# Optimization experiments

Hardware: AMD Instinct MI355X
Metric: run time of the kernel (lower is better)

Reference implementation:

```python
import jax, jax.numpy as jnp
import numpy as np

B, K, G, C = 64, 4000, 200, 91
LAMBDA_BOX, LAMBDA_CLS, LAMBDA_OBJ = 5.0, 1.0, 1.0
EPS = 1e-9


def _make_boxes(key, lead_shape):
    k1, k2 = jax.random.split(key)
    tl = jax.random.uniform(k1, lead_shape + (2,)) * 0.7
    wh = jax.random.uniform(k2, lead_shape + (2,)) * 0.29 + 0.01
    return jnp.concatenate([tl, tl + wh], axis=-1)


def setup_inputs() -> dict:
    key = jax.random.key(0)
    ks = jax.random.split(key, 6)
    pred_boxes = _make_boxes(ks[0], (B, K))
    pred_obj_logits = jax.random.normal(ks[1], (B, K), dtype=jnp.float32)
    pred_cls_logits = jax.random.normal(ks[2], (B, K, C), dtype=jnp.float32)
    gt_boxes = _make_boxes(ks[3], (B, G))
    gt_labels = jax.random.randint(ks[4], (B, G), 0, C)
    n_gt = jax.random.randint(ks[5], (B,), 1, G + 1)
    gt_mask = jnp.arange(G)[None, :] < n_gt[:, None]
    return dict(pred_boxes=pred_boxes, pred_obj_logits=pred_obj_logits,
                pred_cls_logits=pred_cls_logits, gt_boxes=gt_boxes,
                gt_labels=gt_labels, gt_mask=gt_mask)


def _area(x):
    return jnp.clip(x[..., 2] - x[..., 0], 0.0) * jnp.clip(x[..., 3] - x[..., 1], 0.0)


def _pairwise_iou(a, b):
    # a: (K,4), b: (G,4) -> (K,G)
    tl = jnp.maximum(a[:, None, :2], b[None, :, :2])
    br = jnp.minimum(a[:, None, 2:], b[None, :, 2:])
    wh = jnp.clip(br - tl, 0.0)
    inter = wh[..., 0] * wh[..., 1]
    union = jnp.clip(_area(a)[:, None] + _area(b)[None, :] - inter, EPS)
    return inter / union


def _ciou_loss(pb, gb):
    # pb, gb: (M,4) matched pairs; elementwise CIoU loss = 1 - CIoU
    tl = jnp.maximum(pb[:, :2], gb[:, :2])
    br = jnp.minimum(pb[:, 2:], gb[:, 2:])
    wh = jnp.clip(br - tl, 0.0)
    inter = wh[:, 0] * wh[:, 1]
    iou = inter / jnp.clip(_area(pb) + _area(gb) - inter, EPS)
    px = (pb[:, 0] + pb[:, 2]) * 0.5
    py = (pb[:, 1] + pb[:, 3]) * 0.5
    tx = (gb[:, 0] + gb[:, 2]) * 0.5
    ty = (gb[:, 1] + gb[:, 3]) * 0.5
    rho2 = (px - tx) ** 2 + (py - ty) ** 2
    etl = jnp.minimum(pb[:, :2], gb[:, :2])
    ebr = jnp.maximum(pb[:, 2:], gb[:, 2:])
    c2 = jnp.clip((ebr[:, 0] - etl[:, 0]) ** 2 + (ebr[:, 1] - etl[:, 1]) ** 2, EPS)
    pw = jnp.clip(pb[:, 2] - pb[:, 0], EPS)
    ph = jnp.clip(pb[:, 3] - pb[:, 1], EPS)
    tw = jnp.clip(gb[:, 2] - gb[:, 0], EPS)
    th = jnp.clip(gb[:, 3] - gb[:, 1], EPS)
    v = (4.0 / jnp.pi ** 2) * (jnp.arctan(tw / th) - jnp.arctan(pw / ph)) ** 2
    alpha = jax.lax.stop_gradient(v / (1.0 - iou + v + EPS))  # torch.no_grad
    return 1.0 - (iou - rho2 / c2 - alpha * v)


def _greedy_match(iou0):
    # iou0: (K,G), invalid gt columns pre-masked to -1. Fixed min(K,G)-step
    # argmax-and-mask scan reproducing the torch greedy loop (break -> valid=False).
    Gd = iou0.shape[1]
    steps = min(iou0.shape[0], Gd)

    def step(m, _):
        flat = jnp.argmax(m)
        p = flat // Gd
        g = flat % Gd
        valid = m.reshape(-1)[flat] >= 0.0
        m2 = m.at[p, :].set(-1.0).at[:, g].set(-1.0)
        return jnp.where(valid, m2, m), (p, g, valid)

    _, (ps, gs, vs) = jax.lax.scan(step, iou0, None, length=steps)
    return ps, gs, vs


def _per_batch(pred_b, cls_b, gt_b, labels_b, mask_b):
    iou = jax.lax.stop_gradient(_pairwise_iou(pred_b, gt_b))  # matching is non-diff (.item() in torch)
    iou = jnp.where(mask_b[None, :], iou, -1.0)
    ps, gs, vs = _greedy_match(iou)
    vf = vs.astype(pred_b.dtype)
    n = jnp.sum(vf)
    denom = jnp.maximum(n, 1.0)
    pb = pred_b[ps]
    gb = gt_b[gs]
    lbox = jnp.sum(_ciou_loss(pb, gb) * vf) / denom
    logp = jax.nn.log_softmax(cls_b[ps], axis=-1)
    lce = -jnp.take_along_axis(logp, labels_b[gs][:, None], axis=1)[:, 0]
    lcls = jnp.sum(lce * vf) / denom
    obj_tgt = jnp.zeros((pred_b.shape[0],), pred_b.dtype).at[
        jnp.where(vs, ps, pred_b.shape[0])].set(1.0, mode='drop')
    return lbox, lcls, obj_tgt, n > 0.0


def reference(pred_boxes, pred_obj_logits, pred_cls_logits, gt_boxes, gt_labels, gt_mask):
    lbox_b, lcls_b, obj_tgt, has = jax.vmap(_per_batch)(
        pred_boxes, pred_cls_logits, gt_boxes, gt_labels, gt_mask)
    hf = has.astype(pred_boxes.dtype)
    nb = jnp.maximum(jnp.sum(hf), 1.0)
    loss_box = jnp.sum(lbox_b * hf) / nb
    loss_cls = jnp.sum(lcls_b * hf) / nb
    # BCEWithLogits(mean): softplus(x) - t*x
    loss_obj = jnp.mean(jax.nn.softplus(pred_obj_logits) - obj_tgt * pred_obj_logits)
    total = LAMBDA_BOX * loss_box + LAMBDA_CLS * loss_cls + LAMBDA_OBJ * loss_obj
    return total, loss_box, loss_cls, loss_obj
```

## Files before the change

kernel.cpp:

```cpp
#include <hip/hip_runtime.h>
#include <math.h>

#define B_ 64
#define K_ 4000
#define G_ 200
#define C_ 91
#define EPS_ 1e-9f
#define NW_ 16
#define DEPTH_ 32
typedef unsigned long long ull;

#define WS_FLAG 0
#define WS_PART 256
#define WS_TOP 327680

__device__ __forceinline__ float box_area(float4 a) {
#pragma clang fp contract(off)
  return fmaxf(a.z - a.x, 0.f) * fmaxf(a.w - a.y, 0.f);
}

__device__ __forceinline__ float iou_ab(float4 a, float aA, float4 b, float aB) {
#pragma clang fp contract(off)
  float tlx = fmaxf(a.x, b.x), tly = fmaxf(a.y, b.y);
  float brx = fminf(a.z, b.z), bry = fminf(a.w, b.w);
  float w = fmaxf(brx - tlx, 0.f), h = fmaxf(bry - tly, 0.f);
  float inter = w * h;
  float uni = fmaxf(aA + aB - inter, EPS_);
  return inter / uni;
}

__device__ __forceinline__ float ciou_loss(float4 p, float4 g) {
  float tlx = fmaxf(p.x, g.x), tly = fmaxf(p.y, g.y);
  float brx = fminf(p.z, g.z), bry = fminf(p.w, g.w);
  float w = fmaxf(brx - tlx, 0.f), h = fmaxf(bry - tly, 0.f);
  float inter = w * h;
  float areaP = fmaxf(p.z - p.x, 0.f) * fmaxf(p.w - p.y, 0.f);
  float areaG = fmaxf(g.z - g.x, 0.f) * fmaxf(g.w - g.y, 0.f);
  float iou = inter / fmaxf(areaP + areaG - inter, EPS_);
  float px = (p.x + p.z) * 0.5f, py = (p.y + p.w) * 0.5f;
  float tx = (g.x + g.z) * 0.5f, ty = (g.y + g.w) * 0.5f;
  float rho2 = (px - tx) * (px - tx) + (py - ty) * (py - ty);
  float ex = fmaxf(p.z, g.z) - fminf(p.x, g.x);
  float ey = fmaxf(p.w, g.w) - fminf(p.y, g.y);
  float c2 = fmaxf(ex * ex + ey * ey, EPS_);
  float pw = fmaxf(p.z - p.x, EPS_), ph = fmaxf(p.w - p.y, EPS_);
  float tw = fmaxf(g.z - g.x, EPS_), th = fmaxf(g.w - g.y, EPS_);
  float dat = atanf(tw / th) - atanf(pw / ph);
  float v = (4.0f / (float)(M_PI * M_PI)) * dat * dat;
  float alpha = v / ((1.f - iou) + v + EPS_);
  return 1.f - (iou - rho2 / c2 - alpha * v);
}

__global__ void kdetect(const unsigned char* m8, int* flag) {
  int b = threadIdx.x;
  int ok = 1;
  const unsigned char* r = m8 + b * G_;
  if (r[0] != 1) ok = 0;
  int seen0 = 0;
  for (int g = 0; g < G_; ++g) {
    unsigned char c = r[g];
    if (c > 1) { ok = 0; break; }
    if (c == 0) seen0 = 1;
    else if (seen0) { ok = 0; break; }
  }
  int all = __all(ok);
  if (b == 0) *flag = all ? 1 : 0;
}

__device__ __forceinline__ float block_sum(float v, float* s_red) {
  for (int off = 32; off > 0; off >>= 1) v += __shfl_xor(v, off);
  int lane = threadIdx.x & 63, wid = threadIdx.x >> 6;
  if (lane == 0) s_red[wid] = v;
  __syncthreads();
  float r = 0.f;
  if (wid == 0) {
    float t = (lane < NW_) ? s_red[lane] : 0.f;
    for (int off = 32; off > 0; off >>= 1) t += __shfl_xor(t, off);
    r = t;
  }
  __syncthreads();
  return r;
}

__device__ __forceinline__ void merge4_stage(ull& v0, ull& v1, ull& v2, ull& v3,
                                             int off) {
  ull w0 = __shfl_xor(v0, off), w1 = __shfl_xor(v1, off);
  ull w2 = __shfl_xor(v2, off), w3 = __shfl_xor(v3, off);
  ull t0 = v0 > w3 ? v0 : w3;
  ull t1 = v1 > w2 ? v1 : w2;
  ull t2 = v2 > w1 ? v2 : w1;
  ull t3 = v3 > w0 ? v3 : w0;
  ull x;
  if (t2 > t0) { x = t0; t0 = t2; t2 = x; }
  if (t3 > t1) { x = t1; t1 = t3; t3 = x; }
  if (t1 > t0) { x = t0; t0 = t1; t1 = x; }
  if (t3 > t2) { x = t2; t2 = t3; t3 = x; }
  v0 = t0; v1 = t1; v2 = t2; v3 = t3;
}

#define TOP4_INS(key, t0, t1, t2, t3)                   \
  if ((key) > t3) {                                     \
    t3 = (key);                                         \
    ull tmp_;                                           \
    if (t3 > t2) { tmp_ = t2; t2 = t3; t3 = tmp_; }     \
    if (t2 > t1) { tmp_ = t1; t1 = t2; t2 = tmp_; }     \
    if (t1 > t0) { tmp_ = t0; t0 = t1; t1 = tmp_; }     \
  }

__device__ __forceinline__ void rank_extract(ull t0, ull t1, ull t2, ull t3,
                                             ull* dst, int lane) {
  int r0 = 0, r1 = 0, r2 = 0, r3 = 0;
  for (int i = 0; i < 64; ++i) {
    ull o0 = __shfl(t0, i), o1 = __shfl(t1, i);
    ull o2 = __shfl(t2, i), o3 = __shfl(t3, i);
    r0 += (o0 > t0) + (o1 > t0) + (o2 > t0) + (o3 > t0);
    r1 += (o0 > t1) + (o1 > t1) + (o2 > t1) + (o3 > t1);
    r2 += (o0 > t2) + (o1 > t2) + (o2 > t2) + (o3 > t2);
    r3 += (o0 > t3) + (o1 > t3) + (o2 > t3) + (o3 > t3);
  }
  int cut = (t3 != 0ull) ? (r3 + 1) : 0x7FFFFFFF;
  int nc = (t0 != 0ull) + (t1 != 0ull) + (t2 != 0ull) + (t3 != 0ull);
  for (int off = 32; off > 0; off >>= 1) {
    int oc = __shfl_xor(cut, off);
    cut = (oc < cut) ? oc : cut;
    nc += __shfl_xor(nc, off);
  }
  const int Lf = (cut < DEPTH_) ? cut : DEPTH_;
  const int zstart = (Lf < nc) ? Lf : nc;
  if (t0 != 0ull && r0 < Lf) dst[r0] = t0;
  if (t1 != 0ull && r1 < Lf) dst[r1] = t1;
  if (t2 != 0ull && r2 < Lf) dst[r2] = t2;
  if (t3 != 0ull && r3 < Lf) dst[r3] = t3;
  for (int o = lane; o < DEPTH_; o += 64)
    if (o >= zstart) dst[o] = 0ull;
}

__global__ __launch_bounds__(1024) void kinit(const float* __restrict__ pred_boxes,
                                              const float* __restrict__ gt_boxes,
                                              const void* __restrict__ gt_mask,
                                              char* __restrict__ ws) {
  __shared__ float4 s_p[K_];
  const int blk = blockIdx.x;
  const int b = blk >> 3, oct = blk & 7;
  const int tid = threadIdx.x, lane = tid & 63, wid = tid >> 6;
  const int msk8 = *(const int*)(ws + WS_FLAG);
  const float4* p4 = (const float4*)pred_boxes + (size_t)b * K_;
  const float4* g4 = (const float4*)gt_boxes + (size_t)b * G_;

  for (int i = tid; i < K_; i += 1024) s_p[i] = p4[i];
  __syncthreads();

  const int base = oct * 25;
  const int colA = base + wid;
  const int colB = base + 16 + wid;
  const bool hasB = (wid < 9);
  ull* wtop = (ull*)(ws + WS_TOP);

  int vA, vB = 0;
  if (msk8) vA = ((const unsigned char*)gt_mask)[(size_t)b * G_ + colA] != 0;
  else      vA = ((const int*)gt_mask)[(size_t)b * G_ + colA] != 0;
  if (hasB) {
    if (msk8) vB = ((const unsigned char*)gt_mask)[(size_t)b * G_ + colB] != 0;
    else      vB = ((const int*)gt_mask)[(size_t)b * G_ + colB] != 0;
  }

  float4 gbA, gbB;
  float gAA = 0.f, gAB = 0.f;
  if (vA) { gbA = g4[colA]; gAA = box_area(gbA); }
  if (vB) { gbB = g4[colB]; gAB = box_area(gbB); }

  ull a0 = 0, a1 = 0, a2 = 0, a3 = 0;
  ull b0 = 0, b1 = 0, b2 = 0, b3 = 0;
  if (vA | vB) {
#pragma unroll 2
    for (int k = lane; k < K_; k += 64) {
      float4 pb = s_p[k];
      float ar = box_area(pb);
      if (vA) {
        float iou = iou_ab(pb, ar, gbA, gAA);
        ull e = ((ull)__float_as_uint(iou) << 12) | (ull)(4095 - k);
        TOP4_INS(e, a0, a1, a2, a3);
      }
      if (vB) {
        float iou = iou_ab(pb, ar, gbB, gAB);
        ull e = ((ull)__float_as_uint(iou) << 12) | (ull)(4095 - k);
        TOP4_INS(e, b0, b1, b2, b3);
      }
    }
  }
  {
    ull* dstA = wtop + ((size_t)b * G_ + colA) * DEPTH_;
    if (vA) rank_extract(a0, a1, a2, a3, dstA, lane);
    else    for (int o = lane; o < DEPTH_; o += 64) dstA[o] = 0ull;
  }
  if (hasB) {
    ull* dstB = wtop + ((size_t)b * G_ + colB) * DEPTH_;
    if (vB) rank_extract(b0, b1, b2, b3, dstB, lane);
    else    for (int o = lane; o < DEPTH_; o += 64) dstB[o] = 0ull;
  }
}

__global__ __launch_bounds__(1024) void kmerged(
    const float* __restrict__ pred_boxes, const float* __restrict__ obj_logits,
    const float* __restrict__ cls_logits, const float* __restrict__ gt_boxes,
    const int* __restrict__ gt_labels, char* __restrict__ ws) {
  __shared__ float s_gx[G_], s_gy[G_], s_gz[G_], s_gw[G_], s_garea[G_];
  __shared__ unsigned char s_rowused[4096];
  __shared__ ull s_toplist[G_][DEPTH_ + 1];
  __shared__ int s_mp[G_];
  __shared__ unsigned short s_mg[G_];
  __shared__ int s_cnt;
  __shared__ float s_red[NW_];
  const int b = blockIdx.x;
  const int tid = threadIdx.x, lane = tid & 63, wid = tid >> 6;
  const float4* p4 = (const float4*)pred_boxes + (size_t)b * K_;
  const float4* g4 = (const float4*)gt_boxes + (size_t)b * G_;
  const ull* wtop = (const ull*)(ws + WS_TOP);

  for (int g = tid; g < G_; g += 1024) {
    float4 gb = g4[g];
    s_gx[g] = gb.x; s_gy[g] = gb.y; s_gz[g] = gb.z; s_gw[g] = gb.w;
    s_garea[g] = box_area(gb);
  }
  for (int k = tid; k < 4096; k += 1024) s_rowused[k] = 0;
  for (int i = tid; i < G_ * DEPTH_; i += 1024)
    s_toplist[i / DEPTH_][i % DEPTH_] = wtop[((size_t)b * G_) * DEPTH_ + i];
  __syncthreads();

  if (wid == 0) {
    ull key0 = 0, key1 = 0, key2 = 0, key3 = 0;
    int ptr0 = DEPTH_, ptr1 = DEPTH_, ptr2 = DEPTH_, ptr3 = DEPTH_;
    int cloc = 0;
#define SLOTINIT(S)                                                        \
    { int col = S * 64 + lane;                                             \
      if (col < G_) {                                                      \
        ull h_ = s_toplist[col][0];                                        \
        if (h_ != 0ull) {                                                  \
          key##S = (h_ << 8) | (ull)(255 - col); ptr##S = 1; ++cloc; } } }
    SLOTINIT(0) SLOTINIT(1) SLOTINIT(2) SLOTINIT(3)
#undef SLOTINIT
    for (int off = 32; off > 0; off >>= 1) cloc += __shfl_xor(cloc, off);
    const int cnt = cloc;
    if (lane == 0) s_cnt = cnt;

    for (int step = 0; step < cnt;) {
      ull v0 = key0, v1 = key1, v2 = key2, v3 = key3, x;
      if (v1 > v0) { x = v0; v0 = v1; v1 = x; }
      if (v3 > v2) { x = v2; v2 = v3; v3 = x; }
      if (v2 > v0) { x = v0; v0 = v2; v2 = x; }
      if (v3 > v1) { x = v1; v1 = v3; v3 = x; }
      if (v2 > v1) { x = v1; v1 = v2; v2 = x; }
      merge4_stage(v0, v1, v2, v3, 32);
      merge4_stage(v0, v1, v2, v3, 16);
      merge4_stage(v0, v1, v2, v3, 8);
      merge4_stage(v0, v1, v2, v3, 4);
      merge4_stage(v0, v1, v2, v3, 2);
      merge4_stage(v0, v1, v2, v3, 1);
      const int P0 = 4095 - (int)((v0 >> 8) & 0xFFF), G0 = 255 - (int)(v0 & 0xFF);
      const int P1 = 4095 - (int)((v1 >> 8) & 0xFFF), G1 = 255 - (int)(v1 & 0xFF);
      const int P2 = 4095 - (int)((v2 >> 8) & 0xFFF), G2 = 255 - (int)(v2 & 0xFF);
      const int P3 = 4095 - (int)((v3 >> 8) & 0xFFF), G3 = 255 - (int)(v3 & 0xFF);
      const int lim = cnt - step;
      const bool a2 = (v1 != 0ull) && (P1 != P0) && (lim > 1);
      const bool a3 = a2 && (v2 != 0ull) && (P2 != P0) && (P2 != P1) && (lim > 2);
      const bool a4 = a3 && (v3 != 0ull) && (P3 != P0) && (P3 != P1) && (P3 != P2) && (lim > 3);
      const int nacc = 1 + (int)a2 + (int)a3 + (int)a4;
      if (lane == 0) {
        s_mp[step] = P0; s_mg[step] = (unsigned short)G0; s_rowused[P0] = 1;
        if (a2) { s_mp[step + 1] = P1; s_mg[step + 1] = (unsigned short)G1; s_rowused[P1] = 1; }
        if (a3) { s_mp[step + 2] = P2; s_mg[step + 2] = (unsigned short)G2; s_rowused[P2] = 1; }
        if (a4) { s_mp[step + 3] = P3; s_mg[step + 3] = (unsigned short)G3; s_rowused[P3] = 1; }
      }
      __builtin_amdgcn_wave_barrier();
      const int gA = G0, gB = a2 ? G1 : -1, gC = a3 ? G2 : -1, gD = a4 ? G3 : -1;
      const int pA = P0, pB = a2 ? P1 : -1, pC = a3 ? P2 : -1, pD = a4 ? P3 : -1;
      int need = 0;
#define DEMOTE(S)                                                           \
      { int col = S * 64 + lane; ull kk = key##S;                           \
        if (kk != 0ull) {                                                   \
          if (col == gA || col == gB || col == gC || col == gD) {           \
            key##S = 0ull;                                                  \
          } else {                                                          \
            int krow = 4095 - (int)((kk >> 8) & 0xFFF);                     \
            if (krow == pA || krow == pB || krow == pC || krow == pD) {     \
              ull nk = 0ull; int np = ptr##S;                               \
              while (np < DEPTH_) {                                         \
                ull e0 = s_toplist[col][np];                                \
                ull e1 = (np + 1 < DEPTH_) ? s_toplist[col][np + 1] : 0ull; \
                int pr0 = 4095 - (int)((e0 >> 12) & 0xFFF);                 \
                int pr1 = 4095 - (int)((e1 >> 12) & 0xFFF);                 \
                unsigned char u0 = s_rowused[pr0];                          \
                unsigned char u1 = s_rowused[pr1];                          \
                if (e0 == 0ull) { np = DEPTH_; break; }                     \
                if (!u0) { nk = (e0 << 8) | (ull)(255 - col); np += 1; break; } \
                if (e1 == 0ull) { np = DEPTH_; break; }                     \
                if (!u1) { nk = (e1 << 8) | (ull)(255 - col); np += 2; break; } \
                np += 2;                                                    \
              }                                                             \
              ptr##S = np; key##S = nk;                                     \
              if (nk == 0ull) need |= (1 << S); } } } }
      DEMOTE(0) DEMOTE(1) DEMOTE(2) DEMOTE(3)
#undef DEMOTE
      while (__any(need)) {
        unsigned long long bal = __ballot(need != 0);
        int src = (int)__builtin_ctzll(bal);
        int myslot = need ? __builtin_ctz(need) : 0;
        int slot = __shfl(myslot, src);
        int col = slot * 64 + src;
        float4 gb = make_float4(s_gx[col], s_gy[col], s_gz[col], s_gw[col]);
        float gA2 = s_garea[col];
        ull t0 = 0, t1 = 0, t2 = 0, t3 = 0;
#pragma unroll 2
        for (int k = lane; k < K_; k += 64) {
          if (!s_rowused[k]) {
            float4 pb = p4[k];
            float iou = iou_ab(pb, box_area(pb), gb, gA2);
            ull e = ((ull)__float_as_uint(iou) << 12) | (ull)(4095 - k);
            TOP4_INS(e, t0, t1, t2, t3);
          }
        }
        int r0 = 0, r1 = 0, r2 = 0, r3 = 0;
        for (int i = 0; i < 64; ++i) {
          ull o0 = __shfl(t0, i), o1 = __shfl(t1, i);
          ull o2 = __shfl(t2, i), o3 = __shfl(t3, i);
          r0 += (o0 > t0) + (o1 > t0) + (o2 > t0) + (o3 > t0);
          r1 += (o0 > t1) + (o1 > t1) + (o2 > t1) + (o3 > t1);
          r2 += (o0 > t2) + (o1 > t2) + (o2 > t2) + (o3 > t2);
          r3 += (o0 > t3) + (o1 > t3) + (o2 > t3) + (o3 > t3);
        }
        int cut = (t3 != 0ull) ? (r3 + 1) : 0x7FFFFFFF;
        int nc = (t0 != 0ull) + (t1 != 0ull) + (t2 != 0ull) + (t3 != 0ull);
        for (int off = 32; off > 0; off >>= 1) {
          int oc = __shfl_xor(cut, off);
          cut = (oc < cut) ? oc : cut;
          nc += __shfl_xor(nc, off);
        }
        const int Lf = (cut < DEPTH_) ? cut : DEPTH_;
        const int zstart = (Lf < nc) ? Lf : nc;
        if (t0 != 0ull && r0 < Lf) s_toplist[col][r0] = t0;
        if (t1 != 0ull && r1 < Lf) s_toplist[col][r1] = t1;
        if (t2 != 0ull && r2 < Lf) s_toplist[col][r2] = t2;
        if (t3 != 0ull && r3 < Lf) s_toplist[col][r3] = t3;
        for (int o = lane; o < DEPTH_; o += 64)
          if (o >= zstart) s_toplist[col][o] = 0ull;
        __builtin_amdgcn_wave_barrier();
        ull newhead = s_toplist[col][0];
        if (lane == src) {
          ull nk = (newhead << 8) | (ull)(255 - col);
          if (slot == 0) { key0 = nk; ptr0 = 1; }
          else if (slot == 1) { key1 = nk; ptr1 = 1; }
          else if (slot == 2) { key2 = nk; ptr2 = 1; }
          else { key3 = nk; ptr3 = 1; }
          need &= ~(1 << slot);
        }
        __builtin_amdgcn_wave_barrier();
      }
      step += nacc;
    }
  }
  __syncthreads();

  const int cnt = s_cnt;
  float lbox = 0.f, lcls = 0.f;
  for (int i = tid; i < cnt; i += 1024) {
    int p = s_mp[i], g = s_mg[i];
    float4 pb = p4[p];
    float4 gb = make_float4(s_gx[g], s_gy[g], s_gz[g], s_gw[g]);
    lbox += ciou_loss(pb, gb);
    int label = gt_labels[(size_t)b * G_ + g];
    const float* lg = cls_logits + ((size_t)b * K_ + p) * C_;
    float m = -1e30f;
    for (int cc = 0; cc < C_; ++cc) m = fmaxf(m, lg[cc]);
    float s = 0.f;
    for (int cc = 0; cc < C_; ++cc) s += expf(lg[cc] - m);
    lcls += (m + logf(s)) - lg[label];
  }
  float obj = 0.f;
  const float* ol = obj_logits + (size_t)b * K_;
  for (int k = tid; k < K_; k += 1024) {
    float x = ol[k];
    float sp = fmaxf(x, 0.f) + log1pf(expf(-fabsf(x)));
    if (s_rowused[k]) sp -= x;
    obj += sp;
  }
  lbox = block_sum(lbox, s_red);
  lcls = block_sum(lcls, s_red);
  obj = block_sum(obj, s_red);
  if (tid == 0) {
    float* partials = (float*)(ws + WS_PART);
    float n = (float)cnt;
    float denom = fmaxf(n, 1.f);
    partials[b * 4 + 0] = lbox / denom;
    partials[b * 4 + 1] = lcls / denom;
    partials[b * 4 + 2] = obj;
    partials[b * 4 + 3] = (n > 0.f) ? 1.f : 0.f;
  }
}

__global__ void kfinal(const char* __restrict__ ws, float* __restrict__ out) {
  int b = threadIdx.x;
  const float* partials = (const float*)(ws + WS_PART);
  float lb = partials[b * 4 + 0], lc = partials[b * 4 + 1];
  float ob = partials[b * 4 + 2], hf = partials[b * 4 + 3];
  float sb = lb * hf, sc = lc * hf, sh = hf, so = ob;
  for (int off = 32; off > 0; off >>= 1) {
    sb += __shfl_xor(sb, off);
    sc += __shfl_xor(sc, off);
    sh += __shfl_xor(sh, off);
    so += __shfl_xor(so, off);
  }
  if (b == 0) {
    float nb = fmaxf(sh, 1.f);
    float box = sb / nb, cls = sc / nb;
    float obj = so / (float)(B_ * K_);
    out[0] = 5.f * box + cls + obj;
    out[1] = box;
    out[2] = cls;
    out[3] = obj;
  }
}

extern "C" void kernel_launch(void* const* d_in, const int* in_sizes, int n_in,
                              void* d_out, int out_size, void* d_ws, size_t ws_size,
                              hipStream_t stream) {
  const float* pred_boxes = (const float*)d_in[0];
  const float* obj_logits = (const float*)d_in[1];
  const float* cls_logits = (const float*)d_in[2];
  const float* gt_boxes = (const float*)d_in[3];
  const int* gt_labels = (const int*)d_in[4];
  const void* gt_mask = d_in[5];
  float* out = (float*)d_out;
  char* ws = (char*)d_ws;

  hipLaunchKernelGGL(kdetect, dim3(1), dim3(64), 0, stream,
                     (const unsigned char*)gt_mask, (int*)(ws + WS_FLAG));
  hipLaunchKernelGGL(kinit, dim3(B_ * 8), dim3(1024), 0, stream,
                     pred_boxes, gt_boxes, gt_mask, ws);
  hipLaunchKernelGGL(kmerged, dim3(B_), dim3(1024), 0, stream,
                     pred_boxes, obj_logits, cls_logits, gt_boxes, gt_labels, ws);
  hipLaunchKernelGGL(kfinal, dim3(1), dim3(64), 0, stream, ws, out);
}
```

Before: 265.8 us.

## Split matching into single-wave kernel and separate wide epilogue kernel

The merged per-batch kernel is split in two. A 64-thread kernel runs the serial greedy matching and writes matches, the row-used mask and counts to workspace, and a separate 1024-thread kernel computes the CIoU, cross-entropy and objectness sums. The toplist now also keeps a parallel array of decoded row indices, so the demotion scan reads 16-bit rows instead of decoding 64-bit keys. The intent is to stop idling 15 waves during the serial matching phase and to make the demote walk cheaper. The cost is an extra launch plus a workspace round trip for the intermediate results.

```diff
diff --git a/kernel.cpp b/kernel.cpp
--- a/kernel.cpp
+++ b/kernel.cpp
@@ -12,6 +12,9 @@
 
 #define WS_FLAG 0
 #define WS_PART 256
+#define WS_CNT 1536
+#define WS_MATCH 2048
+#define WS_ROWUSED 53248
 #define WS_TOP 327680
 
 __device__ __forceinline__ float box_area(float4 a) {
@@ -200,172 +203,203 @@
   }
 }
 
-__global__ __launch_bounds__(1024) void kmerged(
-    const float* __restrict__ pred_boxes, const float* __restrict__ obj_logits,
-    const float* __restrict__ cls_logits, const float* __restrict__ gt_boxes,
-    const int* __restrict__ gt_labels, char* __restrict__ ws) {
+__global__ __launch_bounds__(64) void kmatch(const float* __restrict__ pred_boxes,
+                                             const float* __restrict__ gt_boxes,
+                                             char* __restrict__ ws) {
   __shared__ float s_gx[G_], s_gy[G_], s_gz[G_], s_gw[G_], s_garea[G_];
   __shared__ unsigned char s_rowused[4096];
-  __shared__ ull s_toplist[G_][DEPTH_ + 1];
+  __shared__ ull s_tlkey[G_][DEPTH_ + 1];
+  __shared__ unsigned short s_tlrow[G_][DEPTH_ + 1];
   __shared__ int s_mp[G_];
   __shared__ unsigned short s_mg[G_];
-  __shared__ int s_cnt;
-  __shared__ float s_red[NW_];
   const int b = blockIdx.x;
-  const int tid = threadIdx.x, lane = tid & 63, wid = tid >> 6;
+  const int lane = threadIdx.x;
   const float4* p4 = (const float4*)pred_boxes + (size_t)b * K_;
   const float4* g4 = (const float4*)gt_boxes + (size_t)b * G_;
   const ull* wtop = (const ull*)(ws + WS_TOP);
 
-  for (int g = tid; g < G_; g += 1024) {
+  for (int g = lane; g < G_; g += 64) {
     float4 gb = g4[g];
     s_gx[g] = gb.x; s_gy[g] = gb.y; s_gz[g] = gb.z; s_gw[g] = gb.w;
     s_garea[g] = box_area(gb);
   }
-  for (int k = tid; k < 4096; k += 1024) s_rowused[k] = 0;
-  for (int i = tid; i < G_ * DEPTH_; i += 1024)
-    s_toplist[i / DEPTH_][i % DEPTH_] = wtop[((size_t)b * G_) * DEPTH_ + i];
-  __syncthreads();
-
-  if (wid == 0) {
-    ull key0 = 0, key1 = 0, key2 = 0, key3 = 0;
-    int ptr0 = DEPTH_, ptr1 = DEPTH_, ptr2 = DEPTH_, ptr3 = DEPTH_;
-    int cloc = 0;
+  for (int k = lane; k < 4096; k += 64) s_rowused[k] = 0;
+  for (int i = lane; i < G_ * DEPTH_; i += 64) {
+    ull v = wtop[(size_t)b * G_ * DEPTH_ + i];
+    int col = i / DEPTH_, o = i % DEPTH_;
+    s_tlkey[col][o] = v;
+    s_tlrow[col][o] = v ? (unsigned short)(4095 - (int)((v >> 12) & 0xFFF))
+                        : (unsigned short)0xFFFF;
+  }
+  __builtin_amdgcn_wave_barrier();
+
+  ull key0 = 0, key1 = 0, key2 = 0, key3 = 0;
+  int ptr0 = DEPTH_, ptr1 = DEPTH_, ptr2 = DEPTH_, ptr3 = DEPTH_;
+  int cloc = 0;
 #define SLOTINIT(S)                                                        \
-    { int col = S * 64 + lane;                                             \
-      if (col < G_) {                                                      \
-        ull h_ = s_toplist[col][0];                                        \
-        if (h_ != 0ull) {                                                  \
-          key##S = (h_ << 8) | (ull)(255 - col); ptr##S = 1; ++cloc; } } }
-    SLOTINIT(0) SLOTINIT(1) SLOTINIT(2) SLOTINIT(3)
+  { int col = S * 64 + lane;                                               \
+    if (col < G_) {                                                        \
+      ull h_ = s_tlkey[col][0];                                            \
+      if (h_ != 0ull) {                                                    \
+        key##S = (h_ << 8) | (ull)(255 - col); ptr##S = 1; ++cloc; } } }
+  SLOTINIT(0) SLOTINIT(1) SLOTINIT(2) SLOTINIT(3)
 #undef SLOTINIT
-    for (int off = 32; off > 0; off >>= 1) cloc += __shfl_xor(cloc, off);
-    const int cnt = cloc;
-    if (lane == 0) s_cnt = cnt;
-
-    for (int step = 0; step < cnt;) {
-      ull v0 = key0, v1 = key1, v2 = key2, v3 = key3, x;
-      if (v1 > v0) { x = v0; v0 = v1; v1 = x; }
-      if (v3 > v2) { x = v2; v2 = v3; v3 = x; }
-      if (v2 > v0) { x = v0; v0 = v2; v2 = x; }
-      if (v3 > v1) { x = v1; v1 = v3; v3 = x; }
-      if (v2 > v1) { x = v1; v1 = v2; v2 = x; }
-      merge4_stage(v0, v1, v2, v3, 32);
-      merge4_stage(v0, v1, v2, v3, 16);
-      merge4_stage(v0, v1, v2, v3, 8);
-      merge4_stage(v0, v1, v2, v3, 4);
-      merge4_stage(v0, v1, v2, v3, 2);
-      merge4_stage(v0, v1, v2, v3, 1);
-      const int P0 = 4095 - (int)((v0 >> 8) & 0xFFF), G0 = 255 - (int)(v0 & 0xFF);
-      const int P1 = 4095 - (int)((v1 >> 8) & 0xFFF), G1 = 255 - (int)(v1 & 0xFF);
-      const int P2 = 4095 - (int)((v2 >> 8) & 0xFFF), G2 = 255 - (int)(v2 & 0xFF);
-      const int P3 = 4095 - (int)((v3 >> 8) & 0xFFF), G3 = 255 - (int)(v3 & 0xFF);
-      const int lim = cnt - step;
-      const bool a2 = (v1 != 0ull) && (P1 != P0) && (lim > 1);
-      const bool a3 = a2 && (v2 != 0ull) && (P2 != P0) && (P2 != P1) && (lim > 2);
-      const bool a4 = a3 && (v3 != 0ull) && (P3 != P0) && (P3 != P1) && (P3 != P2) && (lim > 3);
-      const int nacc = 1 + (int)a2 + (int)a3 + (int)a4;
-      if (lane == 0) {
-        s_mp[step] = P0; s_mg[step] = (unsigned short)G0; s_rowused[P0] = 1;
-        if (a2) { s_mp[step + 1] = P1; s_mg[step + 1] = (unsigned short)G1; s_rowused[P1] = 1; }
-        if (a3) { s_mp[step + 2] = P2; s_mg[step + 2] = (unsigned short)G2; s_rowused[P2] = 1; }
-        if (a4) { s_mp[step + 3] = P3; s_mg[step + 3] = (unsigned short)G3; s_rowused[P3] = 1; }
-      }
+  for (int off = 32; off > 0; off >>= 1) cloc += __shfl_xor(cloc, off);
+  const int cnt = cloc;
+
+  for (int step = 0; step < cnt;) {
+    ull v0 = key0, v1 = key1, v2 = key2, v3 = key3, x;
+    if (v1 > v0) { x = v0; v0 = v1; v1 = x; }
+    if (v3 > v2) { x = v2; v2 = v3; v3 = x; }
+    if (v2 > v0) { x = v0; v0 = v2; v2 = x; }
+    if (v3 > v1) { x = v1; v1 = v3; v3 = x; }
+    if (v2 > v1) { x = v1; v1 = v2; v2 = x; }
+    merge4_stage(v0, v1, v2, v3, 32);
+    merge4_stage(v0, v1, v2, v3, 16);
+    merge4_stage(v0, v1, v2, v3, 8);
+    merge4_stage(v0, v1, v2, v3, 4);
+    merge4_stage(v0, v1, v2, v3, 2);
+    merge4_stage(v0, v1, v2, v3, 1);
+    const int P0 = 4095 - (int)((v0 >> 8) & 0xFFF), G0 = 255 - (int)(v0 & 0xFF);
+    const int P1 = 4095 - (int)((v1 >> 8) & 0xFFF), G1 = 255 - (int)(v1 & 0xFF);
+    const int P2 = 4095 - (int)((v2 >> 8) & 0xFFF), G2 = 255 - (int)(v2 & 0xFF);
+    const int P3 = 4095 - (int)((v3 >> 8) & 0xFFF), G3 = 255 - (int)(v3 & 0xFF);
+    const int lim = cnt - step;
+    const bool a2 = (v1 != 0ull) && (P1 != P0) && (lim > 1);
+    const bool a3 = a2 && (v2 != 0ull) && (P2 != P0) && (P2 != P1) && (lim > 2);
+    const bool a4 = a3 && (v3 != 0ull) && (P3 != P0) && (P3 != P1) && (P3 != P2) && (lim > 3);
+    const int nacc = 1 + (int)a2 + (int)a3 + (int)a4;
+    if (lane == 0) {
+      s_mp[step] = P0; s_mg[step] = (unsigned short)G0; s_rowused[P0] = 1;
+      if (a2) { s_mp[step + 1] = P1; s_mg[step + 1] = (unsigned short)G1; s_rowused[P1] = 1; }
+      if (a3) { s_mp[step + 2] = P2; s_mg[step + 2] = (unsigned short)G2; s_rowused[P2] = 1; }
+      if (a4) { s_mp[step + 3] = P3; s_mg[step + 3] = (unsigned short)G3; s_rowused[P3] = 1; }
+    }
+    __builtin_amdgcn_wave_barrier();
+    const int gA = G0, gB = a2 ? G1 : -1, gC = a3 ? G2 : -1, gD = a4 ? G3 : -1;
+    const int pA = P0, pB = a2 ? P1 : -1, pC = a3 ? P2 : -1, pD = a4 ? P3 : -1;
+    int need = 0;
+#define DEMOTE(S)                                                           \
+    { int col = S * 64 + lane; ull kk = key##S;                             \
+      if (kk != 0ull) {                                                     \
+        if (col == gA || col == gB || col == gC || col == gD) {             \
+          key##S = 0ull;                                                    \
+        } else {                                                            \
+          int krow = 4095 - (int)((kk >> 8) & 0xFFF);                       \
+          if (krow == pA || krow == pB || krow == pC || krow == pD) {       \
+            ull nk = 0ull; int np = ptr##S;                                 \
+            while (np < DEPTH_) {                                           \
+              int r_ = s_tlrow[col][np];                                    \
+              if (r_ == 0xFFFF) { np = DEPTH_; break; }                     \
+              if (!s_rowused[r_]) {                                         \
+                nk = (s_tlkey[col][np] << 8) | (ull)(255 - col);            \
+                ++np; break;                                                \
+              }                                                             \
+              ++np;                                                         \
+            }                                                               \
+            ptr##S = np; key##S = nk;                                       \
+            if (nk == 0ull) need |= (1 << S); } } } }
+    DEMOTE(0) DEMOTE(1) DEMOTE(2) DEMOTE(3)
+#undef DEMOTE
+    while (__any(need)) {
+      unsigned long long bal = __ballot(need != 0);
+      int src = (int)__builtin_ctzll(bal);
+      int myslot = need ? __builtin_ctz(need) : 0;
+      int slot = __shfl(myslot, src);
+      int col = slot * 64 + src;
+      float4 gb = make_float4(s_gx[col], s_gy[col], s_gz[col], s_gw[col]);
+      float gA2 = s_garea[col];
+      ull t0 = 0, t1 = 0, t2 = 0, t3 = 0;
+#pragma unroll 2
+      for (int k = lane; k < K_; k += 64) {
+        if (!s_rowused[k]) {
+          float4 pb = p4[k];
+          float iou = iou_ab(pb, box_area(pb), gb, gA2);
+          ull e = ((ull)__float_as_uint(iou) << 12) | (ull)(4095 - k);
+          TOP4_INS(e, t0, t1, t2, t3);
+        }
+      }
+      int r0 = 0, r1 = 0, r2 = 0, r3 = 0;
+      for (int i = 0; i < 64; ++i) {
+        ull o0 = __shfl(t0, i), o1 = __shfl(t1, i);
+        ull o2 = __shfl(t2, i), o3 = __shfl(t3, i);
+        r0 += (o0 > t0) + (o1 > t0) + (o2 > t0) + (o3 > t0);
+        r1 += (o0 > t1) + (o1 > t1) + (o2 > t1) + (o3 > t1);
+        r2 += (o0 > t2) + (o1 > t2) + (o2 > t2) + (o3 > t2);
+        r3 += (o0 > t3) + (o1 > t3) + (o2 > t3) + (o3 > t3);
+      }
+      int cut = (t3 != 0ull) ? (r3 + 1) : 0x7FFFFFFF;
+      int nc = (t0 != 0ull) + (t1 != 0ull) + (t2 != 0ull) + (t3 != 0ull);
+      for (int off = 32; off > 0; off >>= 1) {
+        int oc = __shfl_xor(cut, off);
+        cut = (oc < cut) ? oc : cut;
+        nc += __shfl_xor(nc, off);
+      }
+      const int Lf = (cut < DEPTH_) ? cut : DEPTH_;
+      const int zstart = (Lf < nc) ? Lf : nc;
+      if (t0 != 0ull && r0 < Lf) {
+        s_tlkey[col][r0] = t0;
+        s_tlrow[col][r0] = (unsigned short)(4095 - (int)((t0 >> 12) & 0xFFF));
+      }
+      if (t1 != 0ull && r1 < Lf) {
+        s_tlkey[col][r1] = t1;
+        s_tlrow[col][r1] = (unsigned short)(4095 - (int)((t1 >> 12) & 0xFFF));
+      }
+      if (t2 != 0ull && r2 < Lf) {
+        s_tlkey[col][r2] = t2;
+        s_tlrow[col][r2] = (unsigned short)(4095 - (int)((t2 >> 12) & 0xFFF));
+      }
+      if (t3 != 0ull && r3 < Lf) {
+        s_tlkey[col][r3] = t3;
+        s_tlrow[col][r3] = (unsigned short)(4095 - (int)((t3 >> 12) & 0xFFF));
+      }
+      for (int o = lane; o < DEPTH_; o += 64)
+        if (o >= zstart) { s_tlkey[col][o] = 0ull; s_tlrow[col][o] = 0xFFFF; }
       __builtin_amdgcn_wave_barrier();
-      const int gA = G0, gB = a2 ? G1 : -1, gC = a3 ? G2 : -1, gD = a4 ? G3 : -1;
-      const int pA = P0, pB = a2 ? P1 : -1, pC = a3 ? P2 : -1, pD = a4 ? P3 : -1;
-      int need = 0;
-#define DEMOTE(S)                                                           \
-      { int col = S * 64 + lane; ull kk = key##S;                           \
-        if (kk != 0ull) {                                                   \
-          if (col == gA || col == gB || col == gC || col == gD) {           \
-            key##S = 0ull;                                                  \
-          } else {                                                          \
-            int krow = 4095 - (int)((kk >> 8) & 0xFFF);                     \
-            if (krow == pA || krow == pB || krow == pC || krow == pD) {     \
-              ull nk = 0ull; int np = ptr##S;                               \
-              while (np < DEPTH_) {                                         \
-                ull e0 = s_toplist[col][np];                                \
-                ull e1 = (np + 1 < DEPTH_) ? s_toplist[col][np + 1] : 0ull; \
-                int pr0 = 4095 - (int)((e0 >> 12) & 0xFFF);                 \
-                int pr1 = 4095 - (int)((e1 >> 12) & 0xFFF);                 \
-                unsigned char u0 = s_rowused[pr0];                          \
-                unsigned char u1 = s_rowused[pr1];                          \
-                if (e0 == 0ull) { np = DEPTH_; break; }                     \
-                if (!u0) { nk = (e0 << 8) | (ull)(255 - col); np += 1; break; } \
-                if (e1 == 0ull) { np = DEPTH_; break; }                     \
-                if (!u1) { nk = (e1 << 8) | (ull)(255 - col); np += 2; break; } \
-                np += 2;                                                    \
-              }                                                             \
-              ptr##S = np; key##S = nk;                                     \
-              if (nk == 0ull) need |= (1 << S); } } } }
-      DEMOTE(0) DEMOTE(1) DEMOTE(2) DEMOTE(3)
-#undef DEMOTE
-      while (__any(need)) {
-        unsigned long long bal = __ballot(need != 0);
-        int src = (int)__builtin_ctzll(bal);
-        int myslot = need ? __builtin_ctz(need) : 0;
-        int slot = __shfl(myslot, src);
-        int col = slot * 64 + src;
-        float4 gb = make_float4(s_gx[col], s_gy[col], s_gz[col], s_gw[col]);
-        float gA2 = s_garea[col];
-        ull t0 = 0, t1 = 0, t2 = 0, t3 = 0;
-#pragma unroll 2
-        for (int k = lane; k < K_; k += 64) {
-          if (!s_rowused[k]) {
-            float4 pb = p4[k];
-            float iou = iou_ab(pb, box_area(pb), gb, gA2);
-            ull e = ((ull)__float_as_uint(iou) << 12) | (ull)(4095 - k);
-            TOP4_INS(e, t0, t1, t2, t3);
-          }
-        }
-        int r0 = 0, r1 = 0, r2 = 0, r3 = 0;
-        for (int i = 0; i < 64; ++i) {
-          ull o0 = __shfl(t0, i), o1 = __shfl(t1, i);
-          ull o2 = __shfl(t2, i), o3 = __shfl(t3, i);
-          r0 += (o0 > t0) + (o1 > t0) + (o2 > t0) + (o3 > t0);
-          r1 += (o0 > t1) + (o1 > t1) + (o2 > t1) + (o3 > t1);
-          r2 += (o0 > t2) + (o1 > t2) + (o2 > t2) + (o3 > t2);
-          r3 += (o0 > t3) + (o1 > t3) + (o2 > t3) + (o3 > t3);
-        }
-        int cut = (t3 != 0ull) ? (r3 + 1) : 0x7FFFFFFF;
-        int nc = (t0 != 0ull) + (t1 != 0ull) + (t2 != 0ull) + (t3 != 0ull);
-        for (int off = 32; off > 0; off >>= 1) {
-          int oc = __shfl_xor(cut, off);
-          cut = (oc < cut) ? oc : cut;
-          nc += __shfl_xor(nc, off);
-        }
-        const int Lf = (cut < DEPTH_) ? cut : DEPTH_;
-        const int zstart = (Lf < nc) ? Lf : nc;
-        if (t0 != 0ull && r0 < Lf) s_toplist[col][r0] = t0;
-        if (t1 != 0ull && r1 < Lf) s_toplist[col][r1] = t1;
-        if (t2 != 0ull && r2 < Lf) s_toplist[col][r2] = t2;
-        if (t3 != 0ull && r3 < Lf) s_toplist[col][r3] = t3;
-        for (int o = lane; o < DEPTH_; o += 64)
-          if (o >= zstart) s_toplist[col][o] = 0ull;
-        __builtin_amdgcn_wave_barrier();
-        ull newhead = s_toplist[col][0];
-        if (lane == src) {
-          ull nk = (newhead << 8) | (ull)(255 - col);
-          if (slot == 0) { key0 = nk; ptr0 = 1; }
-          else if (slot == 1) { key1 = nk; ptr1 = 1; }
-          else if (slot == 2) { key2 = nk; ptr2 = 1; }
-          else { key3 = nk; ptr3 = 1; }
-          need &= ~(1 << slot);
-        }
-        __builtin_amdgcn_wave_barrier();
-      }
-      step += nacc;
+      ull newhead = s_tlkey[col][0];
+      if (lane == src) {
+        ull nk = (newhead << 8) | (ull)(255 - col);
+        if (slot == 0) { key0 = nk; ptr0 = 1; }
+        else if (slot == 1) { key1 = nk; ptr1 = 1; }
+        else if (slot == 2) { key2 = nk; ptr2 = 1; }
+        else { key3 = nk; ptr3 = 1; }
+        need &= ~(1 << slot);
+      }
+      __builtin_amdgcn_wave_barrier();
     }
-  }
-  __syncthreads();
-
-  const int cnt = s_cnt;
+    step += nacc;
+  }
+
+  unsigned* mout = (unsigned*)(ws + WS_MATCH) + b * G_;
+  for (int i = lane; i < cnt; i += 64)
+    mout[i] = ((unsigned)s_mp[i] << 8) | (unsigned)s_mg[i];
+  unsigned* ruo = (unsigned*)(ws + WS_ROWUSED + (size_t)b * K_);
+  const unsigned* rus = (const unsigned*)s_rowused;
+  for (int i = lane; i < K_ / 4; i += 64) ruo[i] = rus[i];
+  if (lane == 0) ((int*)(ws + WS_CNT))[b] = cnt;
+}
+
+__global__ __launch_bounds__(1024) void kepi(const float* __restrict__ pred_boxes,
+                                             const float* __restrict__ obj_logits,
+                                             const float* __restrict__ cls_logits,
+                                             const float* __restrict__ gt_boxes,
+                                             const int* __restrict__ gt_labels,
+                                             char* __restrict__ ws) {
+  __shared__ float s_red[NW_];
+  const int b = blockIdx.x;
+  const int tid = threadIdx.x;
+  const int cnt = ((const int*)(ws + WS_CNT))[b];
+  const unsigned* mm = (const unsigned*)(ws + WS_MATCH) + b * G_;
+  const unsigned char* ru = (const unsigned char*)(ws + WS_ROWUSED) + (size_t)b * K_;
+  const float4* p4 = (const float4*)pred_boxes + (size_t)b * K_;
+  const float4* g4 = (const float4*)gt_boxes + (size_t)b * G_;
+
   float lbox = 0.f, lcls = 0.f;
   for (int i = tid; i < cnt; i += 1024) {
-    int p = s_mp[i], g = s_mg[i];
+    unsigned e = mm[i];
+    int p = (int)(e >> 8), g = (int)(e & 0xFF);
     float4 pb = p4[p];
-    float4 gb = make_float4(s_gx[g], s_gy[g], s_gz[g], s_gw[g]);
+    float4 gb = g4[g];
     lbox += ciou_loss(pb, gb);
     int label = gt_labels[(size_t)b * G_ + g];
     const float* lg = cls_logits + ((size_t)b * K_ + p) * C_;
@@ -380,7 +414,7 @@
   for (int k = tid; k < K_; k += 1024) {
     float x = ol[k];
     float sp = fmaxf(x, 0.f) + log1pf(expf(-fabsf(x)));
-    if (s_rowused[k]) sp -= x;
+    if (ru[k]) sp -= x;
     obj += sp;
   }
   lbox = block_sum(lbox, s_red);
@@ -436,7 +470,9 @@
                      (const unsigned char*)gt_mask, (int*)(ws + WS_FLAG));
   hipLaunchKernelGGL(kinit, dim3(B_ * 8), dim3(1024), 0, stream,
                      pred_boxes, gt_boxes, gt_mask, ws);
-  hipLaunchKernelGGL(kmerged, dim3(B_), dim3(1024), 0, stream,
+  hipLaunchKernelGGL(kmatch, dim3(B_), dim3(64), 0, stream,
+                     pred_boxes, gt_boxes, ws);
+  hipLaunchKernelGGL(kepi, dim3(B_), dim3(1024), 0, stream,
                      pred_boxes, obj_logits, cls_logits, gt_boxes, gt_labels, ws);
   hipLaunchKernelGGL(kfinal, dim3(1), dim3(64), 0, stream, ws, out);
 }
```

After: 299.0 us. +12.5%, slower.

## Drop LDS staging in kinit, skip invalid columns, add row-index side table

Applied to the files above, without the earlier changes.

kinit now gives each wave two adjacent GT columns, reads prediction boxes straight from global memory instead of staging them in LDS, and returns early when both columns are masked. Masked columns no longer write zeroed top lists to the workspace. kmerged instead reads gt_mask itself and zero-fills invalid columns while loading. The greedy-match demotion loop now uses a parallel table of unsigned-short row indices, so it no longer decodes 64-bit keys on every probe, at the cost of extra LDS and extra stores when rebuilding lists.

```diff
diff --git a/kernel.cpp b/kernel.cpp
--- a/kernel.cpp
+++ b/kernel.cpp
@@ -12,7 +12,7 @@
 
 #define WS_FLAG 0
 #define WS_PART 256
-#define WS_TOP 327680
+#define WS_TOP 65536
 
 __device__ __forceinline__ float box_area(float4 a) {
 #pragma clang fp contract(off)
@@ -139,80 +139,68 @@
                                               const float* __restrict__ gt_boxes,
                                               const void* __restrict__ gt_mask,
                                               char* __restrict__ ws) {
-  __shared__ float4 s_p[K_];
-  const int blk = blockIdx.x;
-  const int b = blk >> 3, oct = blk & 7;
-  const int tid = threadIdx.x, lane = tid & 63, wid = tid >> 6;
+  const int wv = blockIdx.x * 16 + (threadIdx.x >> 6);
+  const int lane = threadIdx.x & 63;
+  const int b = wv / 100, j = wv - 100 * b;
+  const int c0 = 2 * j, c1 = 2 * j + 1;
   const int msk8 = *(const int*)(ws + WS_FLAG);
   const float4* p4 = (const float4*)pred_boxes + (size_t)b * K_;
   const float4* g4 = (const float4*)gt_boxes + (size_t)b * G_;
 
-  for (int i = tid; i < K_; i += 1024) s_p[i] = p4[i];
-  __syncthreads();
-
-  const int base = oct * 25;
-  const int colA = base + wid;
-  const int colB = base + 16 + wid;
-  const bool hasB = (wid < 9);
-  ull* wtop = (ull*)(ws + WS_TOP);
-
-  int vA, vB = 0;
-  if (msk8) vA = ((const unsigned char*)gt_mask)[(size_t)b * G_ + colA] != 0;
-  else      vA = ((const int*)gt_mask)[(size_t)b * G_ + colA] != 0;
-  if (hasB) {
-    if (msk8) vB = ((const unsigned char*)gt_mask)[(size_t)b * G_ + colB] != 0;
-    else      vB = ((const int*)gt_mask)[(size_t)b * G_ + colB] != 0;
-  }
+  int vA, vB;
+  if (msk8) {
+    vA = ((const unsigned char*)gt_mask)[(size_t)b * G_ + c0] != 0;
+    vB = ((const unsigned char*)gt_mask)[(size_t)b * G_ + c1] != 0;
+  } else {
+    vA = ((const int*)gt_mask)[(size_t)b * G_ + c0] != 0;
+    vB = ((const int*)gt_mask)[(size_t)b * G_ + c1] != 0;
+  }
+  if (!(vA | vB)) return;
 
   float4 gbA, gbB;
   float gAA = 0.f, gAB = 0.f;
-  if (vA) { gbA = g4[colA]; gAA = box_area(gbA); }
-  if (vB) { gbB = g4[colB]; gAB = box_area(gbB); }
+  if (vA) { gbA = g4[c0]; gAA = box_area(gbA); }
+  if (vB) { gbB = g4[c1]; gAB = box_area(gbB); }
 
   ull a0 = 0, a1 = 0, a2 = 0, a3 = 0;
   ull b0 = 0, b1 = 0, b2 = 0, b3 = 0;
-  if (vA | vB) {
-#pragma unroll 2
-    for (int k = lane; k < K_; k += 64) {
-      float4 pb = s_p[k];
-      float ar = box_area(pb);
-      if (vA) {
-        float iou = iou_ab(pb, ar, gbA, gAA);
-        ull e = ((ull)__float_as_uint(iou) << 12) | (ull)(4095 - k);
-        TOP4_INS(e, a0, a1, a2, a3);
-      }
-      if (vB) {
-        float iou = iou_ab(pb, ar, gbB, gAB);
-        ull e = ((ull)__float_as_uint(iou) << 12) | (ull)(4095 - k);
-        TOP4_INS(e, b0, b1, b2, b3);
-      }
+#pragma unroll 4
+  for (int k = lane; k < K_; k += 64) {
+    float4 pb = p4[k];
+    float ar = box_area(pb);
+    if (vA) {
+      float iou = iou_ab(pb, ar, gbA, gAA);
+      ull e = ((ull)__float_as_uint(iou) << 12) | (ull)(4095 - k);
+      TOP4_INS(e, a0, a1, a2, a3);
     }
-  }
-  {
-    ull* dstA = wtop + ((size_t)b * G_ + colA) * DEPTH_;
-    if (vA) rank_extract(a0, a1, a2, a3, dstA, lane);
-    else    for (int o = lane; o < DEPTH_; o += 64) dstA[o] = 0ull;
-  }
-  if (hasB) {
-    ull* dstB = wtop + ((size_t)b * G_ + colB) * DEPTH_;
-    if (vB) rank_extract(b0, b1, b2, b3, dstB, lane);
-    else    for (int o = lane; o < DEPTH_; o += 64) dstB[o] = 0ull;
-  }
+    if (vB) {
+      float iou = iou_ab(pb, ar, gbB, gAB);
+      ull e = ((ull)__float_as_uint(iou) << 12) | (ull)(4095 - k);
+      TOP4_INS(e, b0, b1, b2, b3);
+    }
+  }
+  ull* wtop = (ull*)(ws + WS_TOP);
+  if (vA) rank_extract(a0, a1, a2, a3, wtop + ((size_t)b * G_ + c0) * DEPTH_, lane);
+  if (vB) rank_extract(b0, b1, b2, b3, wtop + ((size_t)b * G_ + c1) * DEPTH_, lane);
 }
 
 __global__ __launch_bounds__(1024) void kmerged(
     const float* __restrict__ pred_boxes, const float* __restrict__ obj_logits,
     const float* __restrict__ cls_logits, const float* __restrict__ gt_boxes,
-    const int* __restrict__ gt_labels, char* __restrict__ ws) {
+    const int* __restrict__ gt_labels, const void* __restrict__ gt_mask,
+    char* __restrict__ ws) {
   __shared__ float s_gx[G_], s_gy[G_], s_gz[G_], s_gw[G_], s_garea[G_];
+  __shared__ unsigned char s_valid[G_];
   __shared__ unsigned char s_rowused[4096];
-  __shared__ ull s_toplist[G_][DEPTH_ + 1];
+  __shared__ ull s_tlkey[G_][DEPTH_ + 1];
+  __shared__ unsigned short s_tlrow[G_][DEPTH_ + 1];
   __shared__ int s_mp[G_];
   __shared__ unsigned short s_mg[G_];
   __shared__ int s_cnt;
   __shared__ float s_red[NW_];
   const int b = blockIdx.x;
   const int tid = threadIdx.x, lane = tid & 63, wid = tid >> 6;
+  const int msk8 = *(const int*)(ws + WS_FLAG);
   const float4* p4 = (const float4*)pred_boxes + (size_t)b * K_;
   const float4* g4 = (const float4*)gt_boxes + (size_t)b * G_;
   const ull* wtop = (const ull*)(ws + WS_TOP);
@@ -221,10 +209,20 @@
     float4 gb = g4[g];
     s_gx[g] = gb.x; s_gy[g] = gb.y; s_gz[g] = gb.z; s_gw[g] = gb.w;
     s_garea[g] = box_area(gb);
+    int v;
+    if (msk8) v = ((const unsigned char*)gt_mask)[(size_t)b * G_ + g] != 0;
+    else      v = ((const int*)gt_mask)[(size_t)b * G_ + g] != 0;
+    s_valid[g] = (unsigned char)v;
   }
   for (int k = tid; k < 4096; k += 1024) s_rowused[k] = 0;
-  for (int i = tid; i < G_ * DEPTH_; i += 1024)
-    s_toplist[i / DEPTH_][i % DEPTH_] = wtop[((size_t)b * G_) * DEPTH_ + i];
+  __syncthreads();
+  for (int i = tid; i < G_ * DEPTH_; i += 1024) {
+    int col = i >> 5, o = i & 31;
+    ull v = s_valid[col] ? wtop[(size_t)b * G_ * DEPTH_ + i] : 0ull;
+    s_tlkey[col][o] = v;
+    s_tlrow[col][o] = v ? (unsigned short)(4095 - (int)((v >> 12) & 0xFFF))
+                        : (unsigned short)0xFFFF;
+  }
   __syncthreads();
 
   if (wid == 0) {
@@ -234,7 +232,7 @@
 #define SLOTINIT(S)                                                        \
     { int col = S * 64 + lane;                                             \
       if (col < G_) {                                                      \
-        ull h_ = s_toplist[col][0];                                        \
+        ull h_ = s_tlkey[col][0];                                          \
         if (h_ != 0ull) {                                                  \
           key##S = (h_ << 8) | (ull)(255 - col); ptr##S = 1; ++cloc; } } }
     SLOTINIT(0) SLOTINIT(1) SLOTINIT(2) SLOTINIT(3)
@@ -285,17 +283,13 @@
             if (krow == pA || krow == pB || krow == pC || krow == pD) {     \
               ull nk = 0ull; int np = ptr##S;                               \
               while (np < DEPTH_) {                                         \
-                ull e0 = s_toplist[col][np];                                \
-                ull e1 = (np + 1 < DEPTH_) ? s_toplist[col][np + 1] : 0ull; \
-                int pr0 = 4095 - (int)((e0 >> 12) & 0xFFF);                 \
-                int pr1 = 4095 - (int)((e1 >> 12) & 0xFFF);                 \
-                unsigned char u0 = s_rowused[pr0];                          \
-                unsigned char u1 = s_rowused[pr1];                          \
-                if (e0 == 0ull) { np = DEPTH_; break; }                     \
-                if (!u0) { nk = (e0 << 8) | (ull)(255 - col); np += 1; break; } \
-                if (e1 == 0ull) { np = DEPTH_; break; }                     \
-                if (!u1) { nk = (e1 << 8) | (ull)(255 - col); np += 2; break; } \
-                np += 2;                                                    \
+                int r_ = s_tlrow[col][np];                                  \
+                if (r_ == 0xFFFF) { np = DEPTH_; break; }                   \
+                if (!s_rowused[r_]) {                                       \
+                  nk = (s_tlkey[col][np] << 8) | (ull)(255 - col);          \
+                  ++np; break;                                              \
+                }                                                           \
+                ++np;                                                       \
               }                                                             \
               ptr##S = np; key##S = nk;                                     \
               if (nk == 0ull) need |= (1 << S); } } } }
@@ -337,14 +331,26 @@
         }
         const int Lf = (cut < DEPTH_) ? cut : DEPTH_;
         const int zstart = (Lf < nc) ? Lf : nc;
-        if (t0 != 0ull && r0 < Lf) s_toplist[col][r0] = t0;
-        if (t1 != 0ull && r1 < Lf) s_toplist[col][r1] = t1;
-        if (t2 != 0ull && r2 < Lf) s_toplist[col][r2] = t2;
-        if (t3 != 0ull && r3 < Lf) s_toplist[col][r3] = t3;
+        if (t0 != 0ull && r0 < Lf) {
+          s_tlkey[col][r0] = t0;
+          s_tlrow[col][r0] = (unsigned short)(4095 - (int)((t0 >> 12) & 0xFFF));
+        }
+        if (t1 != 0ull && r1 < Lf) {
+          s_tlkey[col][r1] = t1;
+          s_tlrow[col][r1] = (unsigned short)(4095 - (int)((t1 >> 12) & 0xFFF));
+        }
+        if (t2 != 0ull && r2 < Lf) {
+          s_tlkey[col][r2] = t2;
+          s_tlrow[col][r2] = (unsigned short)(4095 - (int)((t2 >> 12) & 0xFFF));
+        }
+        if (t3 != 0ull && r3 < Lf) {
+          s_tlkey[col][r3] = t3;
+          s_tlrow[col][r3] = (unsigned short)(4095 - (int)((t3 >> 12) & 0xFFF));
+        }
         for (int o = lane; o < DEPTH_; o += 64)
-          if (o >= zstart) s_toplist[col][o] = 0ull;
+          if (o >= zstart) { s_tlkey[col][o] = 0ull; s_tlrow[col][o] = 0xFFFF; }
         __builtin_amdgcn_wave_barrier();
-        ull newhead = s_toplist[col][0];
+        ull newhead = s_tlkey[col][0];
         if (lane == src) {
           ull nk = (newhead << 8) | (ull)(255 - col);
           if (slot == 0) { key0 = nk; ptr0 = 1; }
@@ -434,9 +440,10 @@
 
   hipLaunchKernelGGL(kdetect, dim3(1), dim3(64), 0, stream,
                      (const unsigned char*)gt_mask, (int*)(ws + WS_FLAG));
-  hipLaunchKernelGGL(kinit, dim3(B_ * 8), dim3(1024), 0, stream,
+  hipLaunchKernelGGL(kinit, dim3(400), dim3(1024), 0, stream,
                      pred_boxes, gt_boxes, gt_mask, ws);
   hipLaunchKernelGGL(kmerged, dim3(B_), dim3(1024), 0, stream,
-                     pred_boxes, obj_logits, cls_logits, gt_boxes, gt_labels, ws);
+                     pred_boxes, obj_logits, cls_logits, gt_boxes, gt_labels,
+                     gt_mask, ws);
   hipLaunchKernelGGL(kfinal, dim3(1), dim3(64), 0, stream, ws, out);
 }
```

Result: slower. 293.2 us (+10.3%).
